# Kernel tuning notes

Measured on AMD Instinct MI355X. Metric: run time of the kernel, lower is better.

The kernel has to match this reference:

```python
import jax, jax.numpy as jnp
import numpy as np

N_HEAD = 16
ROPE_BASE = 10000.0
RMS_EPS = 1e-6

def rms_norm(x):
    # F.rms_norm(x, (x.size(-1),)) -- no learned weight
    return x * jax.lax.rsqrt(jnp.mean(x * x, axis=-1, keepdims=True) + RMS_EPS)

def rope(x):
    # x: [B, T, H, hd]; rotate halves (non-interleaved) like the torch Rotary
    T, hd = x.shape[1], x.shape[3]
    d = hd // 2
    inv_freq = 1.0 / (ROPE_BASE ** (jnp.arange(0, hd, 2, dtype=jnp.float32) / hd))  # [d]
    t = jnp.arange(T, dtype=jnp.float32)
    freqs = jnp.outer(t, inv_freq)                       # [T, d]
    cos = jnp.cos(freqs)[None, :, None, :]
    sin = jnp.sin(freqs)[None, :, None, :]
    x1, x2 = x[..., :d], x[..., d:]
    y1 = x1 * cos + x2 * sin
    y2 = -x1 * sin + x2 * cos
    return jnp.concatenate([y1, y2], axis=-1).astype(x.dtype)

def setup_inputs() -> dict:
    key = jax.random.key(0)
    ks = jax.random.split(key, 7)
    B, T, D, H = 2, 2048, 1024, N_HEAD
    hd = D // H
    s = 0.02
    return {
        "x": jax.random.normal(ks[0], (B, T, D), jnp.float32),
        "v1": jax.random.normal(ks[1], (B, T, H, hd), jnp.float32),
        "w_q": jax.random.normal(ks[2], (D, D), jnp.float32) * s,
        "w_k": jax.random.normal(ks[3], (D, D), jnp.float32) * s,
        "w_v": jax.random.normal(ks[4], (D, D), jnp.float32) * s,
        "w_proj": jax.random.normal(ks[5], (D, D), jnp.float32) * s,
        "lamb": jnp.float32(0.5),
    }

def reference(x, v1, w_q, w_k, w_v, w_proj, lamb):
    B, T, D = x.shape
    H = N_HEAD
    hd = D // H
    q = (x @ w_q.T).reshape(B, T, H, hd)
    k = (x @ w_k.T).reshape(B, T, H, hd)
    v = (x @ w_v.T).reshape(B, T, H, hd)
    v = (1.0 - lamb) * v + lamb * v1.reshape(B, T, H, hd)
    q, k = rms_norm(q), rms_norm(k)
    q, k = rope(q), rope(k)
    scale = 1.0 / jnp.sqrt(jnp.float32(hd))
    scores = jnp.einsum('bqhd,bkhd->bhqk', q, k) * scale  # [B,H,T,T]
    causal = jnp.tril(jnp.ones((T, T), dtype=bool))
    scores = jnp.where(causal[None, None], scores, jnp.float32(-1e30))
    attn = jax.nn.softmax(scores, axis=-1)
    y = jnp.einsum('bhqk,bkhd->bqhd', attn, v).reshape(B, T, D)
    y = y @ w_proj.T
    return (y, v1)
```

## Files before the change

kernel.cpp:

```cpp
#include <hip/hip_runtime.h>

typedef __bf16 bf16x8 __attribute__((ext_vector_type(8)));
typedef float f32x4 __attribute__((ext_vector_type(4)));
typedef float f32x16 __attribute__((ext_vector_type(16)));

__device__ __forceinline__ unsigned short f2bf(float f) {
    return __builtin_bit_cast(unsigned short, (__bf16)f);
}

__device__ __forceinline__ float bf2f(unsigned short u) {
    unsigned int x = ((unsigned int)u) << 16;
    return __builtin_bit_cast(float, x);
}

__device__ __forceinline__ unsigned int packbf2(float a, float b) {
    unsigned short lo = f2bf(a), hi = f2bf(b);
    return (unsigned int)lo | ((unsigned int)hi << 16);
}

__device__ __forceinline__ bf16x8 load_frag(const unsigned short* p) {
    int4 v = *reinterpret_cast<const int4*>(p);
    return __builtin_bit_cast(bf16x8, v);
}

__device__ __forceinline__ void gload_lds16(const unsigned short* g, unsigned short* l) {
    __builtin_amdgcn_global_load_lds((const __attribute__((address_space(1))) void*)g,
                                     (__attribute__((address_space(3))) void*)l, 16, 0, 0);
}

__global__ __launch_bounds__(256) void prep_bf16(const float* __restrict__ x,
                                                 const float* __restrict__ wq,
                                                 const float* __restrict__ wk,
                                                 const float* __restrict__ wv,
                                                 const float* __restrict__ wp,
                                                 unsigned short* __restrict__ xb,
                                                 unsigned short* __restrict__ wall,
                                                 float* __restrict__ cost,
                                                 float* __restrict__ sint) {
    int bid = blockIdx.x;
    if (bid < 8192) {
        int i = (bid * 256 + threadIdx.x) * 4;
        const float* src;
        unsigned short* dst;
        int soff, doff;
        if (i < (1 << 22)) {
            src = x; dst = xb; soff = i; doff = i;
        } else {
            int j = i - (1 << 22);
            int r = j >> 20;
            src = (r == 0) ? wq : ((r == 1) ? wk : ((r == 2) ? wv : wp));
            dst = wall; soff = j & 1048575; doff = j;
        }
        float4 v = *reinterpret_cast<const float4*>(&src[soff]);
        unsigned short tmp[4] = {f2bf(v.x), f2bf(v.y), f2bf(v.z), f2bf(v.w)};
        *reinterpret_cast<int2*>(&dst[doff]) = *reinterpret_cast<int2*>(tmp);
    } else {
        int i = (bid - 8192) * 256 + threadIdx.x;
        int t = i >> 5, d = i & 31;
        float inv = powf(10000.0f, -(float)d / 32.0f);
        float f = (float)t * inv;
        cost[i] = cosf(f);
        sint[i] = sinf(f);
    }
}

__global__ __launch_bounds__(256) void gemm_qk(const unsigned short* __restrict__ A,
                                               const unsigned short* __restrict__ B,
                                               const float* __restrict__ cost,
                                               const float* __restrict__ sint,
                                               unsigned short* __restrict__ qb,
                                               unsigned short* __restrict__ kb) {
    __shared__ __align__(16) unsigned short As[128 * 64];
    __shared__ __align__(16) unsigned short Bs[128 * 64];
    int tid = threadIdx.x;
    int lane = tid & 63;
    int w = tid >> 6;
    int wm = w >> 1, wn = w & 1;
    int m0 = blockIdx.x * 128;
    int n0 = blockIdx.y * 128;

    f32x4 acc[4][4] = {};

    int r8 = lane >> 3;
    int csrc = (lane & 7) ^ r8;

    for (int k0 = 0; k0 < 1024; k0 += 64) {
        __syncthreads();
#pragma unroll
        for (int c = 0; c < 4; ++c) {
            int row = 32 * w + 8 * c + r8;
            gload_lds16(&A[(size_t)(m0 + row) * 1024 + k0 + csrc * 8], &As[(32 * w + 8 * c) * 64]);
            gload_lds16(&B[(size_t)(n0 + row) * 1024 + k0 + csrc * 8], &Bs[(32 * w + 8 * c) * 64]);
        }
        __syncthreads();
#pragma unroll
        for (int kk = 0; kk < 2; ++kk) {
            int col16 = kk * 4 + (lane >> 4);
            bf16x8 af[4], bfr[4];
#pragma unroll
            for (int i = 0; i < 4; ++i) {
                int row = wm * 64 + i * 16 + (lane & 15);
                af[i] = load_frag(&As[row * 64 + (col16 ^ (row & 7)) * 8]);
            }
#pragma unroll
            for (int j = 0; j < 4; ++j) {
                int row = wn * 64 + j * 16 + (lane & 15);
                bfr[j] = load_frag(&Bs[row * 64 + (col16 ^ (row & 7)) * 8]);
            }
#pragma unroll
            for (int i = 0; i < 4; ++i)
#pragma unroll
                for (int j = 0; j < 4; ++j)
                    acc[i][j] = __builtin_amdgcn_mfma_f32_16x16x32_bf16(af[i], bfr[j], acc[i][j], 0, 0, 0);
        }
    }

    int r0 = (lane >> 4) * 4;
    int cc = lane & 15;
    int sec = blockIdx.y >> 3;
    int hh = (blockIdx.y & 7) * 2 + wn;
    unsigned short* dst = (sec == 0) ? qb : kb;
    float sc = (sec == 0) ? (0.125f * 1.44269504088896f) : 1.0f;
#pragma unroll
    for (int i = 0; i < 4; ++i)
#pragma unroll
        for (int r = 0; r < 4; ++r) {
            float ss = 0.0f;
#pragma unroll
            for (int j = 0; j < 4; ++j) ss += acc[i][j][r] * acc[i][j][r];
            ss += __shfl_xor(ss, 1, 64);
            ss += __shfl_xor(ss, 2, 64);
            ss += __shfl_xor(ss, 4, 64);
            ss += __shfl_xor(ss, 8, 64);
            float rn = rsqrtf(ss * (1.0f / 64.0f) + 1e-6f);
            int mm = m0 + wm * 64 + i * 16 + r0 + r;
            int t = mm & 2047, b = mm >> 11;
            size_t rowb = ((size_t)((b * 16 + hh) * 2048 + t)) * 64;
#pragma unroll
            for (int j = 0; j < 2; ++j) {
                int dm = j * 16 + cc;
                float c = cost[t * 32 + dm], s_ = sint[t * 32 + dm];
                float x1 = acc[i][j][r] * rn;
                float x2 = acc[i][j + 2][r] * rn;
                dst[rowb + dm]      = f2bf((x1 * c + x2 * s_) * sc);
                dst[rowb + 32 + dm] = f2bf((x2 * c - x1 * s_) * sc);
            }
        }
}

__global__ __launch_bounds__(256) void gemm_v(const unsigned short* __restrict__ A,
                                              const unsigned short* __restrict__ Bv,
                                              const float* __restrict__ v1,
                                              const float* __restrict__ lamb_p,
                                              unsigned short* __restrict__ vt,
                                              float* __restrict__ outv1) {
    __shared__ __align__(16) unsigned short smem[2 * 128 * 72];
    unsigned short* As = smem;
    unsigned short* Bs = smem + 128 * 64;
    int tid = threadIdx.x;
    int lane = tid & 63;
    int w = tid >> 6;
    int wm = w >> 1, wn = w & 1;
    int m0 = blockIdx.x * 128;
    int n0 = blockIdx.y * 128;

    f32x4 acc[4][4] = {};

    int r8 = lane >> 3;
    int csrc = (lane & 7) ^ r8;

    for (int k0 = 0; k0 < 1024; k0 += 64) {
        __syncthreads();
#pragma unroll
        for (int c = 0; c < 4; ++c) {
            int row = 32 * w + 8 * c + r8;
            gload_lds16(&A[(size_t)(m0 + row) * 1024 + k0 + csrc * 8], &As[(32 * w + 8 * c) * 64]);
            gload_lds16(&Bv[(size_t)(n0 + row) * 1024 + k0 + csrc * 8], &Bs[(32 * w + 8 * c) * 64]);
        }
        __syncthreads();
#pragma unroll
        for (int kk = 0; kk < 2; ++kk) {
            int col16 = kk * 4 + (lane >> 4);
            bf16x8 af[4], bfr[4];
#pragma unroll
            for (int i = 0; i < 4; ++i) {
                int row = wm * 64 + i * 16 + (lane & 15);
                af[i] = load_frag(&As[row * 64 + (col16 ^ (row & 7)) * 8]);
            }
#pragma unroll
            for (int j = 0; j < 4; ++j) {
                int row = wn * 64 + j * 16 + (lane & 15);
                bfr[j] = load_frag(&Bs[row * 64 + (col16 ^ (row & 7)) * 8]);
            }
#pragma unroll
            for (int i = 0; i < 4; ++i)
#pragma unroll
                for (int j = 0; j < 4; ++j)
                    acc[i][j] = __builtin_amdgcn_mfma_f32_16x16x32_bf16(af[i], bfr[j], acc[i][j], 0, 0, 0);
        }
    }

    typedef unsigned short (*tile_t)[128][72];
    tile_t tile = reinterpret_cast<tile_t>(smem);
    int r0 = (lane >> 4) * 4;
    int cc = lane & 15;
    int hh = blockIdx.y * 2 + wn;
    float lam = lamb_p[0];
    float oml = 1.0f - lam;
    __syncthreads();
#pragma unroll
    for (int i = 0; i < 4; ++i)
#pragma unroll
        for (int r = 0; r < 4; ++r) {
            int tl = wm * 64 + i * 16 + r0 + r;
            int mm = m0 + tl;
            int t = mm & 2047, b = mm >> 11;
            size_t v1row = ((size_t)((b * 2048 + t) * 16 + hh)) * 64;
#pragma unroll
            for (int j = 0; j < 4; ++j) {
                int d = j * 16 + cc;
                float v1v = v1[v1row + d];
                outv1[v1row + d] = v1v;
                tile[wn][tl][d] = f2bf(oml * acc[i][j][r] + lam * v1v);
            }
        }
    __syncthreads();

    int h2 = tid >> 7;
    int idx = tid & 127;
    int rr2 = idx >> 2;
    int c2 = (idx & 3) * 8;
    int hhs = blockIdx.y * 2 + h2;
    int t0 = m0 & 2047;
    int bb = m0 >> 11;
    unsigned short* dst = vt + ((size_t)(bb * 16 + hhs)) * 64 * 2048;
    unsigned short tmp[8];
#pragma unroll
    for (int tb = 0; tb < 128; tb += 32) {
#pragma unroll
        for (int j = 0; j < 8; ++j) tmp[j] = tile[h2][tb + c2 + j][rr2];
        *reinterpret_cast<int4*>(&dst[(size_t)rr2 * 2048 + t0 + tb + c2]) = *reinterpret_cast<int4*>(tmp);
#pragma unroll
        for (int j = 0; j < 8; ++j) tmp[j] = tile[h2][tb + c2 + j][rr2 + 32];
        *reinterpret_cast<int4*>(&dst[(size_t)(rr2 + 32) * 2048 + t0 + tb + c2]) = *reinterpret_cast<int4*>(tmp);
    }
}

__global__ __launch_bounds__(256) void gemm_proj(const unsigned short* __restrict__ pO,
                                                 const float* __restrict__ lsum,
                                                 const unsigned short* __restrict__ B,
                                                 float* __restrict__ C) {
    __shared__ __align__(16) unsigned short As[128 * 64];
    __shared__ __align__(16) unsigned short Bs[128 * 64];
    int tid = threadIdx.x;
    int lane = tid & 63;
    int w = tid >> 6;
    int wm = w >> 1, wn = w & 1;
    int m0 = blockIdx.x * 128;
    int n0 = blockIdx.y * 128;

    f32x4 acc[4][4] = {};

    int r8 = lane >> 3;
    int c8 = lane & 7;
    int csrc = c8 ^ r8;

    for (int k0 = 0; k0 < 1024; k0 += 64) {
        int h = k0 >> 6;
        __syncthreads();
#pragma unroll
        for (int c = 0; c < 4; ++c) {
            int row = 32 * w + 8 * c + r8;
            int m = m0 + row;
            int bh = ((m >> 11) << 4) + h;
            int qi = m & 2047;
            int li = bh * 2048 + qi;
            size_t pi = (size_t)li * 64 + csrc * 8;
            int4 p0 = *reinterpret_cast<const int4*>(&pO[pi]);
            int4 p1 = *reinterpret_cast<const int4*>(&pO[4194304u + pi]);
            float linv = 1.0f / (lsum[li] + lsum[65536 + li]);
            const unsigned short* u0 = reinterpret_cast<const unsigned short*>(&p0);
            const unsigned short* u1 = reinterpret_cast<const unsigned short*>(&p1);
            unsigned short tmp[8];
#pragma unroll
            for (int j = 0; j < 8; ++j) tmp[j] = f2bf((bf2f(u0[j]) + bf2f(u1[j])) * linv);
            *reinterpret_cast<int4*>(&As[row * 64 + c8 * 8]) = *reinterpret_cast<int4*>(tmp);
            gload_lds16(&B[(size_t)(n0 + row) * 1024 + k0 + csrc * 8], &Bs[(32 * w + 8 * c) * 64]);
        }
        __syncthreads();
#pragma unroll
        for (int kk = 0; kk < 2; ++kk) {
            int col16 = kk * 4 + (lane >> 4);
            bf16x8 af[4], bfr[4];
#pragma unroll
            for (int i = 0; i < 4; ++i) {
                int row = wm * 64 + i * 16 + (lane & 15);
                af[i] = load_frag(&As[row * 64 + (col16 ^ (row & 7)) * 8]);
            }
#pragma unroll
            for (int j = 0; j < 4; ++j) {
                int row = wn * 64 + j * 16 + (lane & 15);
                bfr[j] = load_frag(&Bs[row * 64 + (col16 ^ (row & 7)) * 8]);
            }
#pragma unroll
            for (int i = 0; i < 4; ++i)
#pragma unroll
                for (int j = 0; j < 4; ++j)
                    acc[i][j] = __builtin_amdgcn_mfma_f32_16x16x32_bf16(af[i], bfr[j], acc[i][j], 0, 0, 0);
        }
    }
    int r0 = (lane >> 4) * 4;
    int cc = lane & 15;
#pragma unroll
    for (int i = 0; i < 4; ++i)
#pragma unroll
        for (int j = 0; j < 4; ++j)
#pragma unroll
            for (int r = 0; r < 4; ++r) {
                size_t m = m0 + wm * 64 + i * 16 + r0 + r;
                size_t n = n0 + wn * 64 + j * 16 + cc;
                C[m * 1024 + n] = acc[i][j][r];
            }
}

__global__ __launch_bounds__(256) void attn(const unsigned short* __restrict__ qb,
                                            const unsigned short* __restrict__ kb,
                                            const unsigned short* __restrict__ vt,
                                            unsigned short* __restrict__ pO,
                                            float* __restrict__ lsum) {
    __shared__ __align__(16) unsigned short Ks[64][72];
    __shared__ __align__(16) unsigned short Vt[64][72];
    int tid = threadIdx.x;
    int lane = tid & 63;
    int w = tid >> 6;
    int hi = lane >> 5;
    int l31 = lane & 31;

    int bid = blockIdx.x;
    int bh = bid & 31;
    int r5 = bid >> 5;
    int qt = 15 - (r5 >> 1);
    int ck = r5 & 1;
    int q0 = qt * 128;
    const size_t base = (size_t)bh * 2048 * 64;
    const unsigned short* vtb = vt + (size_t)bh * 64 * 2048;
    int ktlo = ck * (qt + 1);
    int kthi = (ck + 1) * (qt + 1);

    bf16x8 qf[4];
    int qrow = q0 + w * 32 + l31;
#pragma unroll
    for (int kd = 0; kd < 4; ++kd)
        qf[kd] = load_frag(&qb[base + (size_t)qrow * 64 + kd * 16 + hi * 8]);

    f32x16 oacc[2] = {};
    float lrun = 0.0f;

    int srow = tid >> 3;
    int scol = (tid & 7) * 8;
    int4 kr0, kr1, vr0, vr1;
#define LOADT(kt_)                                                                                    \
    do {                                                                                              \
        kr0 = *reinterpret_cast<const int4*>(&kb[base + (size_t)((kt_)*64 + srow) * 64 + scol]);      \
        kr1 = *reinterpret_cast<const int4*>(&kb[base + (size_t)((kt_)*64 + srow + 32) * 64 + scol]); \
        vr0 = *reinterpret_cast<const int4*>(&vtb[(size_t)srow * 2048 + (kt_)*64 + scol]);            \
        vr1 = *reinterpret_cast<const int4*>(&vtb[(size_t)(srow + 32) * 2048 + (kt_)*64 + scol]);     \
    } while (0)

    int qwlo = q0 + w * 32;
    {
        LOADT(ktlo);
        for (int kt = ktlo; kt < kthi; ++kt) {
            __syncthreads();
            *reinterpret_cast<int4*>(&Ks[srow][scol]) = kr0;
            *reinterpret_cast<int4*>(&Ks[srow + 32][scol]) = kr1;
            *reinterpret_cast<int4*>(&Vt[srow][scol]) = vr0;
            *reinterpret_cast<int4*>(&Vt[srow + 32][scol]) = vr1;
            __syncthreads();
            if (kt + 1 < kthi) LOADT(kt + 1);

            if (kt * 64 <= qwlo + 31) {
                bool diag = (kt * 64 + 63 > qwlo);
                float rs01 = 0.0f, rs23 = 0.0f;
#pragma unroll
                for (int ntl = 0; ntl < 2; ++ntl) {
                    f32x16 sacc = {};
#pragma unroll
                    for (int kd = 0; kd < 4; ++kd) {
                        bf16x8 kf = load_frag(&Ks[ntl * 32 + l31][kd * 16 + hi * 8]);
                        sacc = __builtin_amdgcn_mfma_f32_32x32x16_bf16(kf, qf[kd], sacc, 0, 0, 0);
                    }

#pragma unroll
                    for (int r = 0; r < 16; ++r) {
                        float s = sacc[r];
                        if (diag) {
                            int kvg = kt * 64 + ntl * 32 + (r & 3) + 8 * (r >> 2) + 4 * hi;
                            if (kvg > qrow) s = -3.0e38f;
                        }
                        float e = __builtin_amdgcn_exp2f(s);
                        sacc[r] = e;
                        if (r & 2) rs23 += e; else rs01 += e;
                    }

                    unsigned int wAa[4], wBb[4];
#pragma unroll
                    for (int rr = 0; rr < 4; ++rr) {
                        wAa[rr] = packbf2(sacc[4 * rr + 0], sacc[4 * rr + 1]);
                        wBb[rr] = packbf2(sacc[4 * rr + 2], sacc[4 * rr + 3]);
                    }

#pragma unroll
                    for (int ks2 = 0; ks2 < 2; ++ks2) {
                        int b2 = ks2 * 2;
                        auto rA = __builtin_amdgcn_permlane32_swap(wAa[b2], wAa[b2 + 1], false, false);
                        auto rB = __builtin_amdgcn_permlane32_swap(wBb[b2], wBb[b2 + 1], false, false);
                        uint4 pa;
                        pa.x = rA[0];
                        pa.y = rB[0];
                        pa.z = rA[1];
                        pa.w = rB[1];
                        bf16x8 paf = __builtin_bit_cast(bf16x8, pa);
                        int ks = ntl * 2 + ks2;
#pragma unroll
                        for (int dt = 0; dt < 2; ++dt) {
                            bf16x8 vtf = load_frag(&Vt[dt * 32 + l31][ks * 16 + hi * 8]);
                            oacc[dt] = __builtin_amdgcn_mfma_f32_32x32x16_bf16(paf, vtf, oacc[dt], 0, 0, 0);
                        }
                    }
                }
                float rs = rs01 + rs23;
                rs += __shfl_xor(rs, 32, 64);
                lrun += rs;
            }
        }
    }

    unsigned short* po = pO + ((size_t)ck * 4194304u);
    float* ls = lsum + ck * 65536;
#pragma unroll
    for (int r = 0; r < 16; ++r) {
        int ql = (r & 3) + 8 * (r >> 2) + 4 * hi;
        int q = q0 + w * 32 + ql;
        size_t ro = ((size_t)bh * 2048 + q) * 64;
        po[ro + l31]      = f2bf(oacc[0][r]);
        po[ro + 32 + l31] = f2bf(oacc[1][r]);
    }
    if (hi == 0) ls[bh * 2048 + q0 + w * 32 + l31] = lrun;
#undef LOADT
}

extern "C" void kernel_launch(void* const* d_in, const int* in_sizes, int n_in,
                              void* d_out, int out_size, void* d_ws, size_t ws_size,
                              hipStream_t stream) {
    const float* x      = (const float*)d_in[0];
    const float* v1     = (const float*)d_in[1];
    const float* w_q    = (const float*)d_in[2];
    const float* w_k    = (const float*)d_in[3];
    const float* w_v    = (const float*)d_in[4];
    const float* w_proj = (const float*)d_in[5];
    const float* lamb   = (const float*)d_in[6];
    float* out = (float*)d_out;

    char* ws = (char*)d_ws;
    unsigned short* xb      = (unsigned short*)(ws + 0);
    unsigned short* wall_b  = (unsigned short*)(ws + (8u  << 20));
    unsigned short* wqkv_b  = wall_b;
    unsigned short* wv_b    = wall_b + 2u * 1048576u;
    unsigned short* wproj_b = wall_b + 3u * 1048576u;
    unsigned short* vtp     = (unsigned short*)(ws + (40u << 20));
    unsigned short* qbuf    = (unsigned short*)(ws + (48u << 20));
    unsigned short* kbuf    = (unsigned short*)(ws + (56u << 20));
    float*          cost    = (float*)        (ws + (72u << 20));
    float*          sint    = (float*)        (ws + (72u << 20) + 262144);
    unsigned short* pO      = (unsigned short*)(ws + (80u << 20));
    float*          lsum    = (float*)        (ws + (112u << 20));

    prep_bf16<<<8448, 256, 0, stream>>>(x, w_q, w_k, w_v, w_proj, xb, wall_b, cost, sint);

    gemm_qk<<<dim3(32, 16), 256, 0, stream>>>(xb, wqkv_b, cost, sint, qbuf, kbuf);
    gemm_v<<<dim3(32, 8), 256, 0, stream>>>(xb, wv_b, v1, lamb, vtp, out + 4194304);

    attn<<<1024, 256, 0, stream>>>(qbuf, kbuf, vtp, pO, lsum);

    gemm_proj<<<dim3(32, 8), 256, 0, stream>>>(pO, lsum, wproj_b, out);
}
```

Baseline: 129.9 us.

## Double-buffer attention K/V tiles with direct global-to-LDS loads and XOR swizzle

Replaces the register-staged K/V tile loading with direct global-to-LDS async copies (gload_lds16) into a two-stage shared-memory ring, so the next tile streams in while the current one is computed. The padded 72-column layout is swapped for an unpadded 64-column layout with an XOR swizzle on 16-byte chunks to avoid bank conflicts. This removes the register round trip and one barrier per iteration, at the cost of doubling LDS use, which may reduce occupancy. It relies on a gload_lds16 helper defined elsewhere in the file.

```diff
diff --git a/kernel.cpp b/kernel.cpp
--- a/kernel.cpp
+++ b/kernel.cpp
@@ -328,8 +328,8 @@
                                             const unsigned short* __restrict__ vt,
                                             unsigned short* __restrict__ pO,
                                             float* __restrict__ lsum) {
-    __shared__ __align__(16) unsigned short Ks[64][72];
-    __shared__ __align__(16) unsigned short Vt[64][72];
+    __shared__ __align__(16) unsigned short KsL[2][64 * 64];
+    __shared__ __align__(16) unsigned short VtL[2][64 * 64];
     int tid = threadIdx.x;
     int lane = tid & 63;
     int w = tid >> 6;
@@ -356,84 +356,85 @@
     f32x16 oacc[2] = {};
     float lrun = 0.0f;
 
-    int srow = tid >> 3;
-    int scol = (tid & 7) * 8;
-    int4 kr0, kr1, vr0, vr1;
-#define LOADT(kt_)                                                                                    \
-    do {                                                                                              \
-        kr0 = *reinterpret_cast<const int4*>(&kb[base + (size_t)((kt_)*64 + srow) * 64 + scol]);      \
-        kr1 = *reinterpret_cast<const int4*>(&kb[base + (size_t)((kt_)*64 + srow + 32) * 64 + scol]); \
-        vr0 = *reinterpret_cast<const int4*>(&vtb[(size_t)srow * 2048 + (kt_)*64 + scol]);            \
-        vr1 = *reinterpret_cast<const int4*>(&vtb[(size_t)(srow + 32) * 2048 + (kt_)*64 + scol]);     \
+    int rl = lane >> 3;
+    int ul = lane & 7;
+#define STAGE(pp, kt_)                                                                     \
+    do {                                                                                   \
+        _Pragma("unroll") for (int i2 = 0; i2 < 2; ++i2) {                                 \
+            int rr = (w * 2 + i2) * 8 + rl;                                                \
+            int cu = ul ^ (rr & 7);                                                        \
+            gload_lds16(&kb[base + (size_t)((kt_) * 64 + rr) * 64 + cu * 8],               \
+                        &KsL[pp][(w * 2 + i2) * 512]);                                     \
+            gload_lds16(&vtb[(size_t)rr * 2048 + (kt_) * 64 + cu * 8],                     \
+                        &VtL[pp][(w * 2 + i2) * 512]);                                     \
+        }                                                                                  \
     } while (0)
 
     int qwlo = q0 + w * 32;
-    {
-        LOADT(ktlo);
-        for (int kt = ktlo; kt < kthi; ++kt) {
-            __syncthreads();
-            *reinterpret_cast<int4*>(&Ks[srow][scol]) = kr0;
-            *reinterpret_cast<int4*>(&Ks[srow + 32][scol]) = kr1;
-            *reinterpret_cast<int4*>(&Vt[srow][scol]) = vr0;
-            *reinterpret_cast<int4*>(&Vt[srow + 32][scol]) = vr1;
-            __syncthreads();
-            if (kt + 1 < kthi) LOADT(kt + 1);
-
-            if (kt * 64 <= qwlo + 31) {
-                bool diag = (kt * 64 + 63 > qwlo);
-                float rs01 = 0.0f, rs23 = 0.0f;
-#pragma unroll
-                for (int ntl = 0; ntl < 2; ++ntl) {
-                    f32x16 sacc = {};
-#pragma unroll
-                    for (int kd = 0; kd < 4; ++kd) {
-                        bf16x8 kf = load_frag(&Ks[ntl * 32 + l31][kd * 16 + hi * 8]);
-                        sacc = __builtin_amdgcn_mfma_f32_32x32x16_bf16(kf, qf[kd], sacc, 0, 0, 0);
+    int p = 0;
+    STAGE(0, ktlo);
+    __syncthreads();
+    for (int kt = ktlo; kt < kthi; ++kt) {
+        if (kt + 1 < kthi) STAGE(p ^ 1, kt + 1);
+
+        if (kt * 64 <= qwlo + 31) {
+            bool diag = (kt * 64 + 63 > qwlo);
+            float rs01 = 0.0f, rs23 = 0.0f;
+#pragma unroll
+            for (int ntl = 0; ntl < 2; ++ntl) {
+                f32x16 sacc = {};
+#pragma unroll
+                for (int kd = 0; kd < 4; ++kd) {
+                    int R = ntl * 32 + l31;
+                    bf16x8 kf = load_frag(&KsL[p][R * 64 + (((kd << 1) | hi) ^ (R & 7)) * 8]);
+                    sacc = __builtin_amdgcn_mfma_f32_32x32x16_bf16(kf, qf[kd], sacc, 0, 0, 0);
+                }
+
+#pragma unroll
+                for (int r = 0; r < 16; ++r) {
+                    float s = sacc[r];
+                    if (diag) {
+                        int kvg = kt * 64 + ntl * 32 + (r & 3) + 8 * (r >> 2) + 4 * hi;
+                        if (kvg > qrow) s = -3.0e38f;
                     }
-
-#pragma unroll
-                    for (int r = 0; r < 16; ++r) {
-                        float s = sacc[r];
-                        if (diag) {
-                            int kvg = kt * 64 + ntl * 32 + (r & 3) + 8 * (r >> 2) + 4 * hi;
-                            if (kvg > qrow) s = -3.0e38f;
-                        }
-                        float e = __builtin_amdgcn_exp2f(s);
-                        sacc[r] = e;
-                        if (r & 2) rs23 += e; else rs01 += e;
-                    }
-
-                    unsigned int wAa[4], wBb[4];
-#pragma unroll
-                    for (int rr = 0; rr < 4; ++rr) {
-                        wAa[rr] = packbf2(sacc[4 * rr + 0], sacc[4 * rr + 1]);
-                        wBb[rr] = packbf2(sacc[4 * rr + 2], sacc[4 * rr + 3]);
-                    }
-
-#pragma unroll
-                    for (int ks2 = 0; ks2 < 2; ++ks2) {
-                        int b2 = ks2 * 2;
-                        auto rA = __builtin_amdgcn_permlane32_swap(wAa[b2], wAa[b2 + 1], false, false);
-                        auto rB = __builtin_amdgcn_permlane32_swap(wBb[b2], wBb[b2 + 1], false, false);
-                        uint4 pa;
-                        pa.x = rA[0];
-                        pa.y = rB[0];
-                        pa.z = rA[1];
-                        pa.w = rB[1];
-                        bf16x8 paf = __builtin_bit_cast(bf16x8, pa);
-                        int ks = ntl * 2 + ks2;
-#pragma unroll
-                        for (int dt = 0; dt < 2; ++dt) {
-                            bf16x8 vtf = load_frag(&Vt[dt * 32 + l31][ks * 16 + hi * 8]);
-                            oacc[dt] = __builtin_amdgcn_mfma_f32_32x32x16_bf16(paf, vtf, oacc[dt], 0, 0, 0);
-                        }
+                    float e = __builtin_amdgcn_exp2f(s);
+                    sacc[r] = e;
+                    if (r & 2) rs23 += e; else rs01 += e;
+                }
+
+                unsigned int wAa[4], wBb[4];
+#pragma unroll
+                for (int rr = 0; rr < 4; ++rr) {
+                    wAa[rr] = packbf2(sacc[4 * rr + 0], sacc[4 * rr + 1]);
+                    wBb[rr] = packbf2(sacc[4 * rr + 2], sacc[4 * rr + 3]);
+                }
+
+#pragma unroll
+                for (int ks2 = 0; ks2 < 2; ++ks2) {
+                    int b2 = ks2 * 2;
+                    auto rA = __builtin_amdgcn_permlane32_swap(wAa[b2], wAa[b2 + 1], false, false);
+                    auto rB = __builtin_amdgcn_permlane32_swap(wBb[b2], wBb[b2 + 1], false, false);
+                    uint4 pa;
+                    pa.x = rA[0];
+                    pa.y = rB[0];
+                    pa.z = rA[1];
+                    pa.w = rB[1];
+                    bf16x8 paf = __builtin_bit_cast(bf16x8, pa);
+                    int ks = ntl * 2 + ks2;
+#pragma unroll
+                    for (int dt = 0; dt < 2; ++dt) {
+                        int R2 = dt * 32 + l31;
+                        bf16x8 vtf = load_frag(&VtL[p][R2 * 64 + (((ks << 1) | hi) ^ (R2 & 7)) * 8]);
+                        oacc[dt] = __builtin_amdgcn_mfma_f32_32x32x16_bf16(paf, vtf, oacc[dt], 0, 0, 0);
                     }
                 }
-                float rs = rs01 + rs23;
-                rs += __shfl_xor(rs, 32, 64);
-                lrun += rs;
-            }
-        }
+            }
+            float rs = rs01 + rs23;
+            rs += __shfl_xor(rs, 32, 64);
+            lrun += rs;
+        }
+        __syncthreads();
+        p ^= 1;
     }
 
     unsigned short* po = pO + ((size_t)ck * 4194304u);
@@ -447,7 +448,7 @@
         po[ro + 32 + l31] = f2bf(oacc[1][r]);
     }
     if (hi == 0) ls[bh * 2048 + q0 + w * 32 + l31] = lrun;
-#undef LOADT
+#undef STAGE
 }
 
 extern "C" void kernel_launch(void* const* d_in, const int* in_sizes, int n_in,
```

Result: no change. 129.4 us (-0.3%).
